# Kernel optimization log

Measured on AMD Instinct MI355X. Metric: run time of the kernel, lower is better.

Reference implementation:

```python
import jax, jax.numpy as jnp
from jax import lax
import numpy as np

PADDING = 1
STRIDE = 1


def setup_inputs() -> dict:
    key = jax.random.key(0)
    k1, k2 = jax.random.split(key)
    x = jax.random.normal(k1, (256, 224, 224), dtype=jnp.float32)       # [C, H, W]
    kernel = jax.random.normal(k2, (256, 256, 3, 3), dtype=jnp.float32)  # [O, C, kh, kw]
    return {"x": x, "kernel": kernel}


def reference(x, kernel):
    # Direct conv2d with zero padding and stride, equivalent to the
    # nested-loop torch implementation (cross-correlation, no bias).
    out = lax.conv_general_dilated(
        x[None],                      # [1, C, H, W]
        kernel,                       # [O, C, kh, kw]
        window_strides=(STRIDE, STRIDE),
        padding=[(PADDING, PADDING), (PADDING, PADDING)],
        dimension_numbers=("NCHW", "OIHW", "NCHW"),
    )
    return out[0]                     # [O, Hout, Wout]
```

## Files before the change

kernel.cpp:

```cpp
#include <hip/hip_runtime.h>
#include <hip/hip_bf16.h>
#include <stdint.h>

#define C_IN  256
#define C_OUT 256
#define H_IN  224
#define W_IN  224
#define HP    226
#define WP    226
#define NPIX  (H_IN * W_IN)
#define BM    128
#define BN    128
#define BK    64

typedef __attribute__((ext_vector_type(8))) short short8;
typedef __attribute__((ext_vector_type(4))) float f32x4;

__device__ __forceinline__ unsigned short f2bf(float f) {
    __hip_bfloat16 b = __float2bfloat16(f);
    return *(unsigned short*)&b;
}

__device__ __forceinline__ void gl_lds16(const unsigned short* g, unsigned short* l) {
    __builtin_amdgcn_global_load_lds(
        (const __attribute__((address_space(1))) unsigned int*)g,
        (__attribute__((address_space(3))) unsigned int*)l,
        16, 0, 0);
}

__global__ void prep_all(const float* __restrict__ x, const float* __restrict__ wk,
                         unsigned short* __restrict__ xp, unsigned short* __restrict__ wb) {
    int b = blockIdx.x;
    int t = threadIdx.x;
    if (b < 3584) {
        int ct = b & 3, wt = (b >> 2) & 3, h = b >> 4;
        int c0 = ct * 64, w0 = wt * 64;
        __shared__ float tile[64][65];
        int w   = t & 63;
        int cl0 = t >> 6;
        #pragma unroll
        for (int i = 0; i < 16; ++i) {
            int cl = i * 4 + cl0;
            float v = 0.f;
            if (w0 + w < W_IN)
                v = x[(size_t)(c0 + cl) * NPIX + (size_t)h * W_IN + w0 + w];
            tile[cl][w] = v;
        }
        __syncthreads();
        int wc = t >> 2;
        int cc = (t & 3) * 16;
        if (w0 + wc < W_IN) {
            uint32_t pk[8];
            #pragma unroll
            for (int j = 0; j < 8; ++j) {
                unsigned short lo = f2bf(tile[cc + 2 * j][wc]);
                unsigned short hi = f2bf(tile[cc + 2 * j + 1][wc]);
                pk[j] = (uint32_t)lo | ((uint32_t)hi << 16);
            }
            size_t base = ((size_t)(h + 1) * WP + (w0 + wc + 1)) * C_IN + c0 + cc;
            uint4* dst = (uint4*)(xp + base);
            dst[0] = make_uint4(pk[0], pk[1], pk[2], pk[3]);
            dst[1] = make_uint4(pk[4], pk[5], pk[6], pk[7]);
        }
        return;
    }
    if (b < 5888) {
        int idx = (b - 3584) * 256 + t;
        int c = idx & 255, o = (idx >> 8) & 255, p = idx >> 16;
        wb[((size_t)p * 256 + o) * 256 + c] = f2bf(wk[((size_t)o * 256 + c) * 9 + p]);
        return;
    }
    int i = (b - 5888) * 256 + t;
    uint4 z = make_uint4(0u, 0u, 0u, 0u);
    if (i < 7232) {
        ((uint4*)xp)[i] = z;
    } else if (i < 14464) {
        ((uint4*)(xp + (size_t)225 * WP * C_IN))[i - 7232] = z;
    } else if (i < 21632) {
        int j = i - 14464; int h = 1 + (j >> 5); int c4 = j & 31;
        ((uint4*)(xp + ((size_t)h * WP) * C_IN))[c4] = z;
    } else if (i < 28800) {
        int j = i - 21632; int h = 1 + (j >> 5); int c4 = j & 31;
        ((uint4*)(xp + ((size_t)h * WP + 225) * C_IN))[c4] = z;
    }
}


__launch_bounds__(256, 3)
__global__ void conv_gemm(const unsigned short* __restrict__ xp,
                          const unsigned short* __restrict__ wb,
                          float* __restrict__ out) {
    int wgid = (blockIdx.x & 7) * 98 + (blockIdx.x >> 3);
    int mt = wgid & 1;
    int nt = wgid >> 1;
    int m0 = mt * BM;
    int n0 = nt * BN;
    int t  = threadIdx.x;
    int l  = t & 63, wv = t >> 6;

    __shared__ __align__(16) unsigned short lds[24576];

    int q8 = ((l & 7) ^ (l >> 3)) * 8;
    int rA = l >> 3;
    int offA0, offA1, offA2, offA3, offB0, offB1, offB2, offB3;
    {
        int r0 = (wv * 4 + 0) * 8 + rA;
        int r1 = (wv * 4 + 1) * 8 + rA;
        int r2 = (wv * 4 + 2) * 8 + rA;
        int r3 = (wv * 4 + 3) * 8 + rA;
        offA0 = (m0 + r0) * C_IN + q8;
        offA1 = (m0 + r1) * C_IN + q8;
        offA2 = (m0 + r2) * C_IN + q8;
        offA3 = (m0 + r3) * C_IN + q8;
        int nc0 = n0 + r0, nc1 = n0 + r1, nc2 = n0 + r2, nc3 = n0 + r3;
        int h0 = nc0 / W_IN, h1 = nc1 / W_IN, h2 = nc2 / W_IN, h3 = nc3 / W_IN;
        offB0 = (h0 * WP + (nc0 - h0 * W_IN)) * C_IN + q8;
        offB1 = (h1 * WP + (nc1 - h1 * W_IN)) * C_IN + q8;
        offB2 = (h2 * WP + (nc2 - h2 * W_IN)) * C_IN + q8;
        offB3 = (h3 * WP + (nc3 - h3 * W_IN)) * C_IN + q8;
    }

    int la = l & 15;
    int lk = l >> 4;
    int mo = (wv >> 1) * 64;
    int no = (wv & 1) * 64;
    int xq0 = ((0 * 4 + lk) ^ (la & 7)) * 8;
    int xq1 = ((1 * 4 + lk) ^ (la & 7)) * 8;

    f32x4 acc[4][4];
    #pragma unroll
    for (int i = 0; i < 4; ++i)
        #pragma unroll
        for (int j = 0; j < 4; ++j)
            acc[i][j] = f32x4{0.f, 0.f, 0.f, 0.f};

#define TAPOFF(S, PV, CSV) int PV = (S) >> 2; int CSV = ((S) & 3) << 6;

#define STAGE_B(BC, S) do {                                                  \
    TAPOFF(S, p_, cs_)                                                       \
    int kh_ = (p_ * 11) >> 5; int kw_ = p_ - 3 * kh_;                        \
    const unsigned short* bS_ = xp + (kh_ * WP + kw_) * C_IN + cs_;          \
    gl_lds16(bS_ + offB0, &lds[8192 + (BC) * 8192 + (wv * 4 + 0) * 512]);    \
    gl_lds16(bS_ + offB1, &lds[8192 + (BC) * 8192 + (wv * 4 + 1) * 512]);    \
    gl_lds16(bS_ + offB2, &lds[8192 + (BC) * 8192 + (wv * 4 + 2) * 512]);    \
    gl_lds16(bS_ + offB3, &lds[8192 + (BC) * 8192 + (wv * 4 + 3) * 512]);    \
} while (0)

#define STAGE_A(S) do {                                                      \
    TAPOFF(S, p_, cs_)                                                       \
    const unsigned short* aS_ = wb + p_ * 65536 + cs_;                       \
    gl_lds16(aS_ + offA0, &lds[(wv * 4 + 0) * 512]);                         \
    gl_lds16(aS_ + offA1, &lds[(wv * 4 + 1) * 512]);                         \
    gl_lds16(aS_ + offA2, &lds[(wv * 4 + 2) * 512]);                         \
    gl_lds16(aS_ + offA3, &lds[(wv * 4 + 3) * 512]);                         \
} while (0)

#define BODY(BC, S, DO_STAGE) do {                                           \
    asm volatile("s_waitcnt vmcnt(0) lgkmcnt(0)" ::: "memory");              \
    __builtin_amdgcn_sched_barrier(0);                                       \
    __builtin_amdgcn_s_barrier();                                            \
    __builtin_amdgcn_sched_barrier(0);                                       \
    if (DO_STAGE) STAGE_B((BC) ^ 1, (S) + 1);                                \
    short8 af_[4][2];                                                        \
    _Pragma("unroll")                                                        \
    for (int i_ = 0; i_ < 4; ++i_) {                                         \
        af_[i_][0] = *(const short8*)&lds[(mo + i_ * 16 + la) * BK + xq0];   \
        af_[i_][1] = *(const short8*)&lds[(mo + i_ * 16 + la) * BK + xq1];   \
    }                                                                        \
    asm volatile("s_waitcnt lgkmcnt(0)" ::: "memory");                       \
    __builtin_amdgcn_sched_barrier(0);                                       \
    __builtin_amdgcn_s_barrier();                                            \
    __builtin_amdgcn_sched_barrier(0);                                       \
    if (DO_STAGE) STAGE_A((S) + 1);                                          \
    short8 b0_[4], b1_[4];                                                   \
    _Pragma("unroll")                                                        \
    for (int i_ = 0; i_ < 4; ++i_) {                                         \
        b0_[i_] = *(const short8*)&lds[8192 + (BC) * 8192 + (no + i_ * 16 + la) * BK + xq0]; \
        b1_[i_] = *(const short8*)&lds[8192 + (BC) * 8192 + (no + i_ * 16 + la) * BK + xq1]; \
    }                                                                        \
    __builtin_amdgcn_s_setprio(1);                                           \
    _Pragma("unroll")                                                        \
    for (int i_ = 0; i_ < 4; ++i_)                                           \
        _Pragma("unroll")                                                    \
        for (int j_ = 0; j_ < 4; ++j_)                                       \
            acc[i_][j_] = __builtin_amdgcn_mfma_f32_16x16x32_bf16(           \
                af_[i_][0], b0_[j_], acc[i_][j_], 0, 0, 0);                  \
    _Pragma("unroll")                                                        \
    for (int i_ = 0; i_ < 4; ++i_)                                           \
        _Pragma("unroll")                                                    \
        for (int j_ = 0; j_ < 4; ++j_)                                       \
            acc[i_][j_] = __builtin_amdgcn_mfma_f32_16x16x32_bf16(           \
                af_[i_][1], b1_[j_], acc[i_][j_], 0, 0, 0);                  \
    __builtin_amdgcn_s_setprio(0);                                           \
} while (0)

    STAGE_B(0, 0);
    STAGE_A(0);
    #pragma unroll 1
    for (int k = 0; k < 17; ++k) {
        BODY(0, 2 * k, 1);
        BODY(1, 2 * k + 1, 1);
    }
    BODY(0, 34, 1);
    BODY(1, 35, 0);

#undef BODY
#undef STAGE_A
#undef STAGE_B
#undef TAPOFF

    int ro = lk * 4;
    #pragma unroll
    for (int i = 0; i < 4; ++i) {
        #pragma unroll
        for (int j = 0; j < 4; ++j) {
            int oo = m0 + mo + i * 16 + ro;
            int nn = n0 + no + j * 16 + la;
            #pragma unroll
            for (int r = 0; r < 4; ++r)
                out[(size_t)(oo + r) * NPIX + nn] = acc[i][j][r];
        }
    }
}

__global__ void conv_naive(const float* __restrict__ x, const float* __restrict__ wk,
                           float* __restrict__ out) {
    int idx = blockIdx.x * 256 + threadIdx.x;
    int n = idx % NPIX;
    int o = idx / NPIX;
    int h = n / W_IN, w = n - (n / W_IN) * W_IN;
    float s = 0.f;
    for (int c = 0; c < C_IN; ++c) {
        const float* xc = x + (size_t)c * NPIX;
        const float* wc = wk + ((size_t)o * C_IN + c) * 9;
        #pragma unroll
        for (int kh = 0; kh < 3; ++kh) {
            int hh = h + kh - 1;
            if (hh < 0 || hh >= H_IN) continue;
            #pragma unroll
            for (int kw = 0; kw < 3; ++kw) {
                int ww = w + kw - 1;
                if (ww < 0 || ww >= W_IN) continue;
                s += xc[hh * W_IN + ww] * wc[kh * 3 + kw];
            }
        }
    }
    out[idx] = s;
}

extern "C" void kernel_launch(void* const* d_in, const int* in_sizes, int n_in,
                              void* d_out, int out_size, void* d_ws, size_t ws_size,
                              hipStream_t stream) {
    const float* x  = (const float*)d_in[0];
    const float* wk = (const float*)d_in[1];
    float* out = (float*)d_out;

    const size_t xp_elems = (size_t)HP * WP * C_IN;
    const size_t wb_elems = (size_t)9 * 256 * 256;
    const size_t need = (xp_elems + wb_elems) * 2;

    if (ws_size < need) {
        conv_naive<<<(C_OUT * NPIX) / 256, 256, 0, stream>>>(x, wk, out);
        return;
    }

    unsigned short* xp = (unsigned short*)d_ws;
    unsigned short* wb = xp + xp_elems;

    prep_all<<<3584 + 2304 + 113, 256, 0, stream>>>(x, wk, xp, wb);
    conv_gemm<<<392 * 2, 256, 0, stream>>>(xp, wb, out);
}
```

Measured before the change: 89.70 us.

## Enlarge conv GEMM tile to 256x256 with 512 threads and prefetch-overlapped staging

Each workgroup now covers all 256 output channels and 256 pixels, using 8 waves, so the weight tile is shared across the whole channel dimension and fewer blocks reload input patches. Both A and B tiles are double-buffered in one staging step that is issued before the compute, with a partial vmcnt wait so the global-to-LDS loads can overlap the MFMA work. The trade-off is a grid of only 196 workgroups, which leaves some CUs idle on a 256-CU part. It also uses about 128KB of LDS per block, limiting occupancy to one block per CU.

```diff
diff --git a/kernel.cpp b/kernel.cpp
--- a/kernel.cpp
+++ b/kernel.cpp
@@ -9,8 +9,8 @@
 #define HP    226
 #define WP    226
 #define NPIX  (H_IN * W_IN)
-#define BM    128
-#define BN    128
+#define BM    256
+#define BN    256
 #define BK    64
 
 typedef __attribute__((ext_vector_type(8))) short short8;
@@ -86,19 +86,16 @@
 }
 
 
-__launch_bounds__(256, 3)
+__launch_bounds__(512, 2)
 __global__ void conv_gemm(const unsigned short* __restrict__ xp,
                           const unsigned short* __restrict__ wb,
                           float* __restrict__ out) {
-    int wgid = (blockIdx.x & 7) * 98 + (blockIdx.x >> 3);
-    int mt = wgid & 1;
-    int nt = wgid >> 1;
-    int m0 = mt * BM;
+    int nt = blockIdx.x;
     int n0 = nt * BN;
     int t  = threadIdx.x;
     int l  = t & 63, wv = t >> 6;
 
-    __shared__ __align__(16) unsigned short lds[24576];
+    __shared__ __align__(16) unsigned short lds[2 * 32768];
 
     int q8 = ((l & 7) ^ (l >> 3)) * 8;
     int rA = l >> 3;
@@ -108,10 +105,10 @@
         int r1 = (wv * 4 + 1) * 8 + rA;
         int r2 = (wv * 4 + 2) * 8 + rA;
         int r3 = (wv * 4 + 3) * 8 + rA;
-        offA0 = (m0 + r0) * C_IN + q8;
-        offA1 = (m0 + r1) * C_IN + q8;
-        offA2 = (m0 + r2) * C_IN + q8;
-        offA3 = (m0 + r3) * C_IN + q8;
+        offA0 = r0 * C_IN + q8;
+        offA1 = r1 * C_IN + q8;
+        offA2 = r2 * C_IN + q8;
+        offA3 = r3 * C_IN + q8;
         int nc0 = n0 + r0, nc1 = n0 + r1, nc2 = n0 + r2, nc3 = n0 + r3;
         int h0 = nc0 / W_IN, h1 = nc1 / W_IN, h2 = nc2 / W_IN, h3 = nc3 / W_IN;
         offB0 = (h0 * WP + (nc0 - h0 * W_IN)) * C_IN + q8;
@@ -122,80 +119,71 @@
 
     int la = l & 15;
     int lk = l >> 4;
-    int mo = (wv >> 1) * 64;
-    int no = (wv & 1) * 64;
+    int wr = wv >> 2;
+    int wc = wv & 3;
+    int mo = wr * 128;
+    int no = wc * 64;
     int xq0 = ((0 * 4 + lk) ^ (la & 7)) * 8;
     int xq1 = ((1 * 4 + lk) ^ (la & 7)) * 8;
 
-    f32x4 acc[4][4];
+    f32x4 acc[8][4];
     #pragma unroll
-    for (int i = 0; i < 4; ++i)
+    for (int i = 0; i < 8; ++i)
         #pragma unroll
         for (int j = 0; j < 4; ++j)
             acc[i][j] = f32x4{0.f, 0.f, 0.f, 0.f};
 
-#define TAPOFF(S, PV, CSV) int PV = (S) >> 2; int CSV = ((S) & 3) << 6;
-
-#define STAGE_B(BC, S) do {                                                  \
-    TAPOFF(S, p_, cs_)                                                       \
+#define STAGE(BD, S) do {                                                    \
+    int s_ = (S);                                                            \
+    int p_ = s_ >> 2, cs_ = (s_ & 3) << 6;                                   \
     int kh_ = (p_ * 11) >> 5; int kw_ = p_ - 3 * kh_;                        \
+    const unsigned short* aS_ = wb + p_ * 65536 + cs_;                       \
     const unsigned short* bS_ = xp + (kh_ * WP + kw_) * C_IN + cs_;          \
-    gl_lds16(bS_ + offB0, &lds[8192 + (BC) * 8192 + (wv * 4 + 0) * 512]);    \
-    gl_lds16(bS_ + offB1, &lds[8192 + (BC) * 8192 + (wv * 4 + 1) * 512]);    \
-    gl_lds16(bS_ + offB2, &lds[8192 + (BC) * 8192 + (wv * 4 + 2) * 512]);    \
-    gl_lds16(bS_ + offB3, &lds[8192 + (BC) * 8192 + (wv * 4 + 3) * 512]);    \
+    gl_lds16(aS_ + offA0, &lds[(BD) * 32768 + (wv * 4 + 0) * 512]);          \
+    gl_lds16(aS_ + offA1, &lds[(BD) * 32768 + (wv * 4 + 1) * 512]);          \
+    gl_lds16(aS_ + offA2, &lds[(BD) * 32768 + (wv * 4 + 2) * 512]);          \
+    gl_lds16(aS_ + offA3, &lds[(BD) * 32768 + (wv * 4 + 3) * 512]);          \
+    gl_lds16(bS_ + offB0, &lds[(BD) * 32768 + 16384 + (wv * 4 + 0) * 512]);  \
+    gl_lds16(bS_ + offB1, &lds[(BD) * 32768 + 16384 + (wv * 4 + 1) * 512]);  \
+    gl_lds16(bS_ + offB2, &lds[(BD) * 32768 + 16384 + (wv * 4 + 2) * 512]);  \
+    gl_lds16(bS_ + offB3, &lds[(BD) * 32768 + 16384 + (wv * 4 + 3) * 512]);  \
 } while (0)
 
-#define STAGE_A(S) do {                                                      \
-    TAPOFF(S, p_, cs_)                                                       \
-    const unsigned short* aS_ = wb + p_ * 65536 + cs_;                       \
-    gl_lds16(aS_ + offA0, &lds[(wv * 4 + 0) * 512]);                         \
-    gl_lds16(aS_ + offA1, &lds[(wv * 4 + 1) * 512]);                         \
-    gl_lds16(aS_ + offA2, &lds[(wv * 4 + 2) * 512]);                         \
-    gl_lds16(aS_ + offA3, &lds[(wv * 4 + 3) * 512]);                         \
-} while (0)
-
-#define BODY(BC, S, DO_STAGE) do {                                           \
-    asm volatile("s_waitcnt vmcnt(0) lgkmcnt(0)" ::: "memory");              \
-    __builtin_amdgcn_sched_barrier(0);                                       \
-    __builtin_amdgcn_s_barrier();                                            \
-    __builtin_amdgcn_sched_barrier(0);                                       \
-    if (DO_STAGE) STAGE_B((BC) ^ 1, (S) + 1);                                \
-    short8 af_[4][2];                                                        \
+#define MFMA_HALF(BC, XQ) do {                                               \
+    short8 af_[8], bf_[4];                                                   \
     _Pragma("unroll")                                                        \
-    for (int i_ = 0; i_ < 4; ++i_) {                                         \
-        af_[i_][0] = *(const short8*)&lds[(mo + i_ * 16 + la) * BK + xq0];   \
-        af_[i_][1] = *(const short8*)&lds[(mo + i_ * 16 + la) * BK + xq1];   \
-    }                                                                        \
+    for (int i_ = 0; i_ < 8; ++i_)                                           \
+        af_[i_] = *(const short8*)&lds[(BC) * 32768 + (mo + i_ * 16 + la) * BK + (XQ)]; \
+    _Pragma("unroll")                                                        \
+    for (int j_ = 0; j_ < 4; ++j_)                                           \
+        bf_[j_] = *(const short8*)&lds[(BC) * 32768 + 16384 + (no + j_ * 16 + la) * BK + (XQ)]; \
     asm volatile("s_waitcnt lgkmcnt(0)" ::: "memory");                       \
     __builtin_amdgcn_sched_barrier(0);                                       \
-    __builtin_amdgcn_s_barrier();                                            \
-    __builtin_amdgcn_sched_barrier(0);                                       \
-    if (DO_STAGE) STAGE_A((S) + 1);                                          \
-    short8 b0_[4], b1_[4];                                                   \
-    _Pragma("unroll")                                                        \
-    for (int i_ = 0; i_ < 4; ++i_) {                                         \
-        b0_[i_] = *(const short8*)&lds[8192 + (BC) * 8192 + (no + i_ * 16 + la) * BK + xq0]; \
-        b1_[i_] = *(const short8*)&lds[8192 + (BC) * 8192 + (no + i_ * 16 + la) * BK + xq1]; \
-    }                                                                        \
     __builtin_amdgcn_s_setprio(1);                                           \
     _Pragma("unroll")                                                        \
-    for (int i_ = 0; i_ < 4; ++i_)                                           \
+    for (int i_ = 0; i_ < 8; ++i_)                                           \
         _Pragma("unroll")                                                    \
         for (int j_ = 0; j_ < 4; ++j_)                                       \
             acc[i_][j_] = __builtin_amdgcn_mfma_f32_16x16x32_bf16(           \
-                af_[i_][0], b0_[j_], acc[i_][j_], 0, 0, 0);                  \
-    _Pragma("unroll")                                                        \
-    for (int i_ = 0; i_ < 4; ++i_)                                           \
-        _Pragma("unroll")                                                    \
-        for (int j_ = 0; j_ < 4; ++j_)                                       \
-            acc[i_][j_] = __builtin_amdgcn_mfma_f32_16x16x32_bf16(           \
-                af_[i_][1], b1_[j_], acc[i_][j_], 0, 0, 0);                  \
+                af_[i_], bf_[j_], acc[i_][j_], 0, 0, 0);                     \
     __builtin_amdgcn_s_setprio(0);                                           \
 } while (0)
 
-    STAGE_B(0, 0);
-    STAGE_A(0);
+#define BODY(BC, S, DO_STAGE) do {                                           \
+    if (DO_STAGE) STAGE((BC) ^ 1, (S) + 1);                                  \
+    asm volatile("s_waitcnt vmcnt(%0)" :: "i"((DO_STAGE) ? 8 : 0) : "memory"); \
+    __builtin_amdgcn_sched_barrier(0);                                       \
+    __builtin_amdgcn_s_barrier();                                            \
+    __builtin_amdgcn_sched_barrier(0);                                       \
+    MFMA_HALF(BC, xq0);                                                      \
+    MFMA_HALF(BC, xq1);                                                      \
+    asm volatile("s_waitcnt lgkmcnt(0)" ::: "memory");                       \
+    __builtin_amdgcn_sched_barrier(0);                                       \
+    __builtin_amdgcn_s_barrier();                                            \
+    __builtin_amdgcn_sched_barrier(0);                                       \
+} while (0)
+
+    STAGE(0, 0);
     #pragma unroll 1
     for (int k = 0; k < 17; ++k) {
         BODY(0, 2 * k, 1);
@@ -205,16 +193,15 @@
     BODY(1, 35, 0);
 
 #undef BODY
-#undef STAGE_A
-#undef STAGE_B
-#undef TAPOFF
+#undef MFMA_HALF
+#undef STAGE
 
     int ro = lk * 4;
     #pragma unroll
-    for (int i = 0; i < 4; ++i) {
+    for (int i = 0; i < 8; ++i) {
         #pragma unroll
         for (int j = 0; j < 4; ++j) {
-            int oo = m0 + mo + i * 16 + ro;
+            int oo = mo + i * 16 + ro;
             int nn = n0 + no + j * 16 + la;
             #pragma unroll
             for (int r = 0; r < 4; ++r)
@@ -268,5 +255,5 @@
     unsigned short* wb = xp + xp_elems;
 
     prep_all<<<3584 + 2304 + 113, 256, 0, stream>>>(x, wk, xp, wb);
-    conv_gemm<<<392 * 2, 256, 0, stream>>>(xp, wb, out);
-}
+    conv_gemm<<<196, 512, 0, stream>>>(xp, wb, out);
+}
```

After: 88.82 us. About the same (-1.0%).

## Halve K tile and double-buffer both operands with partial vmcnt waits

Applied to the files above, without the earlier changes.

Shrinks the K tile from 64 to 32 so both the weight and input tiles fit in a double buffer. The next stage's global-to-LDS loads are issued before waiting on the current buffer, using vmcnt(4) instead of a full drain. The smaller LDS footprint lets occupancy rise to 4 workgroups per CU. The cost is twice as many K iterations, each carrying two barriers, and half as many MFMAs between synchronisations.

```diff
diff --git a/kernel.cpp b/kernel.cpp
--- a/kernel.cpp
+++ b/kernel.cpp
@@ -11,7 +11,7 @@
 #define NPIX  (H_IN * W_IN)
 #define BM    128
 #define BN    128
-#define BK    64
+#define BK    32
 
 typedef __attribute__((ext_vector_type(8))) short short8;
 typedef __attribute__((ext_vector_type(4))) float f32x4;
@@ -86,7 +86,7 @@
 }
 
 
-__launch_bounds__(256, 3)
+__launch_bounds__(256, 4)
 __global__ void conv_gemm(const unsigned short* __restrict__ xp,
                           const unsigned short* __restrict__ wb,
                           float* __restrict__ out) {
@@ -98,34 +98,26 @@
     int t  = threadIdx.x;
     int l  = t & 63, wv = t >> 6;
 
-    __shared__ __align__(16) unsigned short lds[24576];
-
-    int q8 = ((l & 7) ^ (l >> 3)) * 8;
-    int rA = l >> 3;
-    int offA0, offA1, offA2, offA3, offB0, offB1, offB2, offB3;
+    __shared__ __align__(16) unsigned short lds[2 * 8192];
+
+    int lq8 = ((l & 3) ^ ((l >> 2) & 3)) * 8;
+    int offA0, offA1, offB0, offB1;
     {
-        int r0 = (wv * 4 + 0) * 8 + rA;
-        int r1 = (wv * 4 + 1) * 8 + rA;
-        int r2 = (wv * 4 + 2) * 8 + rA;
-        int r3 = (wv * 4 + 3) * 8 + rA;
-        offA0 = (m0 + r0) * C_IN + q8;
-        offA1 = (m0 + r1) * C_IN + q8;
-        offA2 = (m0 + r2) * C_IN + q8;
-        offA3 = (m0 + r3) * C_IN + q8;
-        int nc0 = n0 + r0, nc1 = n0 + r1, nc2 = n0 + r2, nc3 = n0 + r3;
-        int h0 = nc0 / W_IN, h1 = nc1 / W_IN, h2 = nc2 / W_IN, h3 = nc3 / W_IN;
-        offB0 = (h0 * WP + (nc0 - h0 * W_IN)) * C_IN + q8;
-        offB1 = (h1 * WP + (nc1 - h1 * W_IN)) * C_IN + q8;
-        offB2 = (h2 * WP + (nc2 - h2 * W_IN)) * C_IN + q8;
-        offB3 = (h3 * WP + (nc3 - h3 * W_IN)) * C_IN + q8;
+        int r0 = (2 * wv + 0) * 16 + (l >> 2);
+        int r1 = r0 + 16;
+        offA0 = (m0 + r0) * C_IN + lq8;
+        offA1 = (m0 + r1) * C_IN + lq8;
+        int nc0 = n0 + r0, nc1 = n0 + r1;
+        int h0 = nc0 / W_IN, h1 = nc1 / W_IN;
+        offB0 = (h0 * WP + (nc0 - h0 * W_IN)) * C_IN + lq8;
+        offB1 = (h1 * WP + (nc1 - h1 * W_IN)) * C_IN + lq8;
     }
 
     int la = l & 15;
     int lk = l >> 4;
     int mo = (wv >> 1) * 64;
     int no = (wv & 1) * 64;
-    int xq0 = ((0 * 4 + lk) ^ (la & 7)) * 8;
-    int xq1 = ((1 * 4 + lk) ^ (la & 7)) * 8;
+    int xq = (lk ^ (la & 3)) * 8;
 
     f32x4 acc[4][4];
     #pragma unroll
@@ -134,80 +126,63 @@
         for (int j = 0; j < 4; ++j)
             acc[i][j] = f32x4{0.f, 0.f, 0.f, 0.f};
 
-#define TAPOFF(S, PV, CSV) int PV = (S) >> 2; int CSV = ((S) & 3) << 6;
-
-#define STAGE_B(BC, S) do {                                                  \
-    TAPOFF(S, p_, cs_)                                                       \
+#define STAGE(BD, S) do {                                                    \
+    int s_ = (S);                                                            \
+    int p_ = s_ >> 3, cs_ = (s_ & 7) << 5;                                   \
     int kh_ = (p_ * 11) >> 5; int kw_ = p_ - 3 * kh_;                        \
+    const unsigned short* aS_ = wb + p_ * 65536 + cs_;                       \
     const unsigned short* bS_ = xp + (kh_ * WP + kw_) * C_IN + cs_;          \
-    gl_lds16(bS_ + offB0, &lds[8192 + (BC) * 8192 + (wv * 4 + 0) * 512]);    \
-    gl_lds16(bS_ + offB1, &lds[8192 + (BC) * 8192 + (wv * 4 + 1) * 512]);    \
-    gl_lds16(bS_ + offB2, &lds[8192 + (BC) * 8192 + (wv * 4 + 2) * 512]);    \
-    gl_lds16(bS_ + offB3, &lds[8192 + (BC) * 8192 + (wv * 4 + 3) * 512]);    \
+    gl_lds16(aS_ + offA0, &lds[(BD) * 8192 + (2 * wv + 0) * 512]);           \
+    gl_lds16(aS_ + offA1, &lds[(BD) * 8192 + (2 * wv + 1) * 512]);           \
+    gl_lds16(bS_ + offB0, &lds[(BD) * 8192 + 4096 + (2 * wv + 0) * 512]);    \
+    gl_lds16(bS_ + offB1, &lds[(BD) * 8192 + 4096 + (2 * wv + 1) * 512]);    \
 } while (0)
 
-#define STAGE_A(S) do {                                                      \
-    TAPOFF(S, p_, cs_)                                                       \
-    const unsigned short* aS_ = wb + p_ * 65536 + cs_;                       \
-    gl_lds16(aS_ + offA0, &lds[(wv * 4 + 0) * 512]);                         \
-    gl_lds16(aS_ + offA1, &lds[(wv * 4 + 1) * 512]);                         \
-    gl_lds16(aS_ + offA2, &lds[(wv * 4 + 2) * 512]);                         \
-    gl_lds16(aS_ + offA3, &lds[(wv * 4 + 3) * 512]);                         \
-} while (0)
-
-#define BODY(BC, S, DO_STAGE) do {                                           \
-    asm volatile("s_waitcnt vmcnt(0) lgkmcnt(0)" ::: "memory");              \
-    __builtin_amdgcn_sched_barrier(0);                                       \
-    __builtin_amdgcn_s_barrier();                                            \
-    __builtin_amdgcn_sched_barrier(0);                                       \
-    if (DO_STAGE) STAGE_B((BC) ^ 1, (S) + 1);                                \
-    short8 af_[4][2];                                                        \
+#define COMPUTE(BC) do {                                                     \
+    short8 af_[4], bf_[4];                                                   \
     _Pragma("unroll")                                                        \
-    for (int i_ = 0; i_ < 4; ++i_) {                                         \
-        af_[i_][0] = *(const short8*)&lds[(mo + i_ * 16 + la) * BK + xq0];   \
-        af_[i_][1] = *(const short8*)&lds[(mo + i_ * 16 + la) * BK + xq1];   \
-    }                                                                        \
+    for (int i_ = 0; i_ < 4; ++i_)                                           \
+        af_[i_] = *(const short8*)&lds[(BC) * 8192 + (mo + i_ * 16 + la) * BK + xq]; \
+    _Pragma("unroll")                                                        \
+    for (int i_ = 0; i_ < 4; ++i_)                                           \
+        bf_[i_] = *(const short8*)&lds[(BC) * 8192 + 4096 + (no + i_ * 16 + la) * BK + xq]; \
     asm volatile("s_waitcnt lgkmcnt(0)" ::: "memory");                       \
     __builtin_amdgcn_sched_barrier(0);                                       \
-    __builtin_amdgcn_s_barrier();                                            \
-    __builtin_amdgcn_sched_barrier(0);                                       \
-    if (DO_STAGE) STAGE_A((S) + 1);                                          \
-    short8 b0_[4], b1_[4];                                                   \
-    _Pragma("unroll")                                                        \
-    for (int i_ = 0; i_ < 4; ++i_) {                                         \
-        b0_[i_] = *(const short8*)&lds[8192 + (BC) * 8192 + (no + i_ * 16 + la) * BK + xq0]; \
-        b1_[i_] = *(const short8*)&lds[8192 + (BC) * 8192 + (no + i_ * 16 + la) * BK + xq1]; \
-    }                                                                        \
     __builtin_amdgcn_s_setprio(1);                                           \
     _Pragma("unroll")                                                        \
     for (int i_ = 0; i_ < 4; ++i_)                                           \
         _Pragma("unroll")                                                    \
         for (int j_ = 0; j_ < 4; ++j_)                                       \
             acc[i_][j_] = __builtin_amdgcn_mfma_f32_16x16x32_bf16(           \
-                af_[i_][0], b0_[j_], acc[i_][j_], 0, 0, 0);                  \
-    _Pragma("unroll")                                                        \
-    for (int i_ = 0; i_ < 4; ++i_)                                           \
-        _Pragma("unroll")                                                    \
-        for (int j_ = 0; j_ < 4; ++j_)                                       \
-            acc[i_][j_] = __builtin_amdgcn_mfma_f32_16x16x32_bf16(           \
-                af_[i_][1], b1_[j_], acc[i_][j_], 0, 0, 0);                  \
+                af_[i_], bf_[j_], acc[i_][j_], 0, 0, 0);                     \
     __builtin_amdgcn_s_setprio(0);                                           \
 } while (0)
 
-    STAGE_B(0, 0);
-    STAGE_A(0);
+#define BODY(BC, S, DO_STAGE) do {                                           \
+    if (DO_STAGE) STAGE((BC) ^ 1, (S) + 1);                                  \
+    asm volatile("s_waitcnt vmcnt(%0)" :: "i"((DO_STAGE) ? 4 : 0) : "memory"); \
+    __builtin_amdgcn_sched_barrier(0);                                       \
+    __builtin_amdgcn_s_barrier();                                            \
+    __builtin_amdgcn_sched_barrier(0);                                       \
+    COMPUTE(BC);                                                             \
+    asm volatile("s_waitcnt lgkmcnt(0)" ::: "memory");                       \
+    __builtin_amdgcn_sched_barrier(0);                                       \
+    __builtin_amdgcn_s_barrier();                                            \
+    __builtin_amdgcn_sched_barrier(0);                                       \
+} while (0)
+
+    STAGE(0, 0);
     #pragma unroll 1
-    for (int k = 0; k < 17; ++k) {
+    for (int k = 0; k < 35; ++k) {
         BODY(0, 2 * k, 1);
         BODY(1, 2 * k + 1, 1);
     }
-    BODY(0, 34, 1);
-    BODY(1, 35, 0);
+    BODY(0, 70, 1);
+    BODY(1, 71, 0);
 
 #undef BODY
-#undef STAGE_A
-#undef STAGE_B
-#undef TAPOFF
+#undef COMPUTE
+#undef STAGE
 
     int ro = lk * 4;
     #pragma unroll
```

After: 100.2 us. +11.7%, slower.
